# Kernel optimization log

Measured on AMD Instinct MI355X. Metric: run time of the kernel, lower is better.

Reference implementation:

```python
import jax, jax.numpy as jnp
import numpy as np

BETA = 1.0
JITTER = 1e-6


def setup_inputs() -> dict:
    key = jax.random.key(0)
    k1, k2, k3, k4 = jax.random.split(key, 4)
    N, L = 256, 8192
    R_clean = jax.random.normal(k1, (N, L, 3, 3), dtype=jnp.float32)
    t = jax.random.uniform(k2, (N,), dtype=jnp.float32, minval=0.05, maxval=1.0)
    noise = jax.random.normal(k3, (N, L, 3, 3), dtype=jnp.float32)
    eps_noise = jax.random.normal(k4, (N, L, 3, 3), dtype=jnp.float32)
    return {"R_clean": R_clean, "t": t, "noise": noise, "eps_noise": eps_noise}


def _svd_project_so3(F):
    # F: (..., 3, 3).  R = U diag(1,1,det(U V^T)) V^T
    U, S, Vh = jnp.linalg.svd(F, full_matrices=False)
    d = jnp.linalg.det(jnp.matmul(U, Vh))          # (...,)
    mid = jnp.concatenate(
        [jnp.ones(d.shape + (2,), dtype=F.dtype), d[..., None]], axis=-1
    )                                               # (..., 3) = (1, 1, det)
    # U @ diag(mid) @ Vh == (U * mid[..., None, :]) @ Vh
    return jnp.matmul(U * mid[..., None, :], Vh)


def reference(R_clean, t, noise, eps_noise):
    # sample_theta: F_t = alpha_t * R_clean + sqrt(alpha_t) * noise
    alpha_t = (BETA * t).reshape(-1, 1, 1, 1)       # (N,1,1,1)
    F_t = alpha_t * R_clean + jnp.sqrt(alpha_t) * noise
    # svd_project_so3 adds a tiny random jitter before SVD
    F = F_t + JITTER * eps_noise
    return _svd_project_so3(F)
```

## Files before the change

kernel.cpp:

```cpp
#include <hip/hip_runtime.h>

#define TPB  256
#define MPB  256
#define F4PB 576

__device__ __forceinline__ void jrot(float app, float aqq, float apq,
                                     float& c, float& s) {
    float tau = (aqq - app) * 0.5f * __builtin_amdgcn_rcpf(apq);
    float t = __builtin_amdgcn_rcpf(fabsf(tau) +
              __builtin_amdgcn_sqrtf(fmaf(tau, tau, 1.0f)));
    t = copysignf(t, tau);
    t = (fabsf(apq) < 1e-30f) ? 0.0f : t;
    c = __builtin_amdgcn_rsqf(fmaf(t, t, 1.0f));
    s = t * c;
}

__global__ __launch_bounds__(TPB)
void so3_proj_kernel(const float* __restrict__ Rc,
                     const float* __restrict__ Tt,
                     const float* __restrict__ Nz,
                     const float* __restrict__ Ez,
                     float* __restrict__ Out,
                     int L)
{
    __shared__ float4 lds4[F4PB];
    float* lds = (float*)lds4;

    const int tid = threadIdx.x;
    const long long base = (long long)blockIdx.x * MPB;
    const int n = (int)(base / (long long)L);
    const float alpha = Tt[n];
    const float sa = __builtin_amdgcn_sqrtf(alpha);

    const float4* R4 = (const float4*)(Rc + base * 9);
    const float4* N4 = (const float4*)(Nz + base * 9);
    const float4* E4 = (const float4*)(Ez + base * 9);
    float4*       O4 = (float4*)(Out + base * 9);

    #pragma unroll
    for (int it = 0; it < 3; ++it) {
        int j = tid + it * TPB;
        if (j < F4PB) {
            float4 r = R4[j], z = N4[j], e = E4[j];
            float4 f;
            f.x = fmaf(alpha, r.x, fmaf(sa, z.x, 1e-6f * e.x));
            f.y = fmaf(alpha, r.y, fmaf(sa, z.y, 1e-6f * e.y));
            f.z = fmaf(alpha, r.z, fmaf(sa, z.z, 1e-6f * e.z));
            f.w = fmaf(alpha, r.w, fmaf(sa, z.w, 1e-6f * e.w));
            lds4[j] = f;
        }
    }
    __syncthreads();

    float F[9];
    #pragma unroll
    for (int k = 0; k < 9; ++k) F[k] = lds[tid * 9 + k];

    float a00 = F[0]*F[0] + F[3]*F[3] + F[6]*F[6];
    float a01 = F[0]*F[1] + F[3]*F[4] + F[6]*F[7];
    float a02 = F[0]*F[2] + F[3]*F[5] + F[6]*F[8];
    float a11 = F[1]*F[1] + F[4]*F[4] + F[7]*F[7];
    float a12 = F[1]*F[2] + F[4]*F[5] + F[7]*F[8];
    float a22 = F[2]*F[2] + F[5]*F[5] + F[8]*F[8];

    float v00=1.f, v01=0.f, v02=0.f;
    float v10=0.f, v11=1.f, v12=0.f;
    float v20=0.f, v21=0.f, v22=1.f;

    #pragma unroll
    for (int sweep = 0; sweep < 5; ++sweep) {
        float c, s, t0, t1;
        jrot(a00, a11, a01, c, s);
        t0 = c*c*a00 - 2.f*c*s*a01 + s*s*a11;
        t1 = s*s*a00 + 2.f*c*s*a01 + c*c*a11;
        a00 = t0; a11 = t1; a01 = 0.f;
        t0 = c*a02 - s*a12; t1 = s*a02 + c*a12; a02 = t0; a12 = t1;
        t0 = c*v00 - s*v01; v01 = s*v00 + c*v01; v00 = t0;
        t0 = c*v10 - s*v11; v11 = s*v10 + c*v11; v10 = t0;
        t0 = c*v20 - s*v21; v21 = s*v20 + c*v21; v20 = t0;
        jrot(a00, a22, a02, c, s);
        t0 = c*c*a00 - 2.f*c*s*a02 + s*s*a22;
        t1 = s*s*a00 + 2.f*c*s*a02 + c*c*a22;
        a00 = t0; a22 = t1; a02 = 0.f;
        t0 = c*a01 - s*a12; t1 = s*a01 + c*a12; a01 = t0; a12 = t1;
        t0 = c*v00 - s*v02; v02 = s*v00 + c*v02; v00 = t0;
        t0 = c*v10 - s*v12; v12 = s*v10 + c*v12; v10 = t0;
        t0 = c*v20 - s*v22; v22 = s*v20 + c*v22; v20 = t0;
        jrot(a11, a22, a12, c, s);
        t0 = c*c*a11 - 2.f*c*s*a12 + s*s*a22;
        t1 = s*s*a11 + 2.f*c*s*a12 + c*c*a22;
        a11 = t0; a22 = t1; a12 = 0.f;
        t0 = c*a01 - s*a02; t1 = s*a01 + c*a02; a01 = t0; a02 = t1;
        t0 = c*v01 - s*v02; v02 = s*v01 + c*v02; v01 = t0;
        t0 = c*v11 - s*v12; v12 = s*v11 + c*v12; v11 = t0;
        t0 = c*v21 - s*v22; v22 = s*v21 + c*v22; v21 = t0;
    }

    float l0 = a00, l1 = a11, l2 = a22;
    if (l0 < l1) { float t;
        t=l0;l0=l1;l1=t; t=v00;v00=v01;v01=t; t=v10;v10=v11;v11=t; t=v20;v20=v21;v21=t; }
    if (l0 < l2) { float t;
        t=l0;l0=l2;l2=t; t=v00;v00=v02;v02=t; t=v10;v10=v12;v12=t; t=v20;v20=v22;v22=t; }
    if (l1 < l2) { float t;
        t=l1;l1=l2;l2=t; t=v01;v01=v02;v02=t; t=v11;v11=v12;v12=t; t=v21;v21=v22;v22=t; }

    float v3x = v10*v21 - v20*v11;
    float v3y = v20*v01 - v00*v21;
    float v3z = v00*v11 - v10*v01;

    float u1x = F[0]*v00 + F[1]*v10 + F[2]*v20;
    float u1y = F[3]*v00 + F[4]*v10 + F[5]*v20;
    float u1z = F[6]*v00 + F[7]*v10 + F[8]*v20;
    float inv1 = __builtin_amdgcn_rsqf(fmaxf(u1x*u1x + u1y*u1y + u1z*u1z, 1e-30f));
    u1x *= inv1; u1y *= inv1; u1z *= inv1;

    float wx = F[0]*v01 + F[1]*v11 + F[2]*v21;
    float wy = F[3]*v01 + F[4]*v11 + F[5]*v21;
    float wz = F[6]*v01 + F[7]*v11 + F[8]*v21;
    float dd = u1x*wx + u1y*wy + u1z*wz;
    wx -= dd*u1x; wy -= dd*u1y; wz -= dd*u1z;
    float inv2 = __builtin_amdgcn_rsqf(fmaxf(wx*wx + wy*wy + wz*wz, 1e-30f));
    float u2x = wx*inv2, u2y = wy*inv2, u2z = wz*inv2;

    float u3x = u1y*u2z - u1z*u2y;
    float u3y = u1z*u2x - u1x*u2z;
    float u3z = u1x*u2y - u1y*u2x;

    float Rm[9];
    Rm[0] = u1x*v00 + u2x*v01 + u3x*v3x;
    Rm[1] = u1x*v10 + u2x*v11 + u3x*v3y;
    Rm[2] = u1x*v20 + u2x*v21 + u3x*v3z;
    Rm[3] = u1y*v00 + u2y*v01 + u3y*v3x;
    Rm[4] = u1y*v10 + u2y*v11 + u3y*v3y;
    Rm[5] = u1y*v20 + u2y*v21 + u3y*v3z;
    Rm[6] = u1z*v00 + u2z*v01 + u3z*v3x;
    Rm[7] = u1z*v10 + u2z*v11 + u3z*v3y;
    Rm[8] = u1z*v20 + u2z*v21 + u3z*v3z;

    __syncthreads();
    #pragma unroll
    for (int k = 0; k < 9; ++k) lds[tid * 9 + k] = Rm[k];
    __syncthreads();

    #pragma unroll
    for (int it = 0; it < 3; ++it) {
        int j = tid + it * TPB;
        if (j < F4PB) O4[j] = lds4[j];
    }
}

extern "C" void kernel_launch(void* const* d_in, const int* in_sizes, int n_in,
                              void* d_out, int out_size, void* d_ws, size_t ws_size,
                              hipStream_t stream) {
    const float* Rc = (const float*)d_in[0];
    const float* Tt = (const float*)d_in[1];
    const float* Nz = (const float*)d_in[2];
    const float* Ez = (const float*)d_in[3];
    float* Out = (float*)d_out;

    const long long mats = (long long)in_sizes[0] / 9;
    const int L = (int)(mats / in_sizes[1]);
    const int blocks = (int)(mats / MPB);

    so3_proj_kernel<<<blocks, TPB, 0, stream>>>(Rc, Tt, Nz, Ez, Out, L);
}
```

Before: 250.2 us.

## Simplify Jacobi rotations and exit sweeps early on wavefront convergence

Rewrites the Jacobi rotation to compute tan directly from a numerically stable formula with one rcp, and updates the diagonal entries with the a_pp - t*a_pq identity in place of the full quadratic form. It also drops the full unroll of the sweep loop and adds a wavefront-wide convergence test after sweep 3, so waves whose matrices are already diagonal skip the remaining sweeps. The goal is to cut ALU work in a compute-heavy kernel. The trade-offs are an extra reduction and branch per sweep, and the loss of unrolling.

```diff
diff --git a/kernel.cpp b/kernel.cpp
--- a/kernel.cpp
+++ b/kernel.cpp
@@ -5,12 +5,12 @@
 #define F4PB 576
 
 __device__ __forceinline__ void jrot(float app, float aqq, float apq,
-                                     float& c, float& s) {
-    float tau = (aqq - app) * 0.5f * __builtin_amdgcn_rcpf(apq);
-    float t = __builtin_amdgcn_rcpf(fabsf(tau) +
-              __builtin_amdgcn_sqrtf(fmaf(tau, tau, 1.0f)));
-    t = copysignf(t, tau);
-    t = (fabsf(apq) < 1e-30f) ? 0.0f : t;
+                                     float& c, float& s, float& t) {
+    float d  = aqq - app;
+    float p2 = apq + apq;
+    float rad = __builtin_amdgcn_sqrtf(fmaf(d, d, p2 * p2));
+    float den = fmaxf(fabsf(d) + rad, 1e-38f);
+    t = p2 * copysignf(__builtin_amdgcn_rcpf(den), d);
     c = __builtin_amdgcn_rsqf(fmaf(t, t, 1.0f));
     s = t * c;
 }
@@ -67,33 +67,31 @@
     float v10=0.f, v11=1.f, v12=0.f;
     float v20=0.f, v21=0.f, v22=1.f;
 
-    #pragma unroll
     for (int sweep = 0; sweep < 5; ++sweep) {
-        float c, s, t0, t1;
-        jrot(a00, a11, a01, c, s);
-        t0 = c*c*a00 - 2.f*c*s*a01 + s*s*a11;
-        t1 = s*s*a00 + 2.f*c*s*a01 + c*c*a11;
-        a00 = t0; a11 = t1; a01 = 0.f;
-        t0 = c*a02 - s*a12; t1 = s*a02 + c*a12; a02 = t0; a12 = t1;
-        t0 = c*v00 - s*v01; v01 = s*v00 + c*v01; v00 = t0;
-        t0 = c*v10 - s*v11; v11 = s*v10 + c*v11; v10 = t0;
-        t0 = c*v20 - s*v21; v21 = s*v20 + c*v21; v20 = t0;
-        jrot(a00, a22, a02, c, s);
-        t0 = c*c*a00 - 2.f*c*s*a02 + s*s*a22;
-        t1 = s*s*a00 + 2.f*c*s*a02 + c*c*a22;
-        a00 = t0; a22 = t1; a02 = 0.f;
-        t0 = c*a01 - s*a12; t1 = s*a01 + c*a12; a01 = t0; a12 = t1;
-        t0 = c*v00 - s*v02; v02 = s*v00 + c*v02; v00 = t0;
-        t0 = c*v10 - s*v12; v12 = s*v10 + c*v12; v10 = t0;
-        t0 = c*v20 - s*v22; v22 = s*v20 + c*v22; v20 = t0;
-        jrot(a11, a22, a12, c, s);
-        t0 = c*c*a11 - 2.f*c*s*a12 + s*s*a22;
-        t1 = s*s*a11 + 2.f*c*s*a12 + c*c*a22;
-        a11 = t0; a22 = t1; a12 = 0.f;
-        t0 = c*a01 - s*a02; t1 = s*a01 + c*a02; a01 = t0; a02 = t1;
-        t0 = c*v01 - s*v02; v02 = s*v01 + c*v02; v01 = t0;
-        t0 = c*v11 - s*v12; v12 = s*v11 + c*v12; v11 = t0;
-        t0 = c*v21 - s*v22; v22 = s*v21 + c*v22; v21 = t0;
+        if (sweep >= 3) {
+            float off = fmaf(a01, a01, fmaf(a02, a02, a12 * a12));
+            float sc  = fmaf(a00, a00, fmaf(a11, a11, a22 * a22));
+            if (__all(off <= 1e-13f * sc)) break;
+        }
+        float c, s, t, t0;
+        jrot(a00, a11, a01, c, s, t);
+        a00 = fmaf(-t, a01, a00); a11 = fmaf(t, a01, a11); a01 = 0.f;
+        t0 = c*a02 - s*a12; a12 = fmaf(s, a02, c*a12); a02 = t0;
+        t0 = c*v00 - s*v01; v01 = fmaf(s, v00, c*v01); v00 = t0;
+        t0 = c*v10 - s*v11; v11 = fmaf(s, v10, c*v11); v10 = t0;
+        t0 = c*v20 - s*v21; v21 = fmaf(s, v20, c*v21); v20 = t0;
+        jrot(a00, a22, a02, c, s, t);
+        a00 = fmaf(-t, a02, a00); a22 = fmaf(t, a02, a22); a02 = 0.f;
+        t0 = c*a01 - s*a12; a12 = fmaf(s, a01, c*a12); a01 = t0;
+        t0 = c*v00 - s*v02; v02 = fmaf(s, v00, c*v02); v00 = t0;
+        t0 = c*v10 - s*v12; v12 = fmaf(s, v10, c*v12); v10 = t0;
+        t0 = c*v20 - s*v22; v22 = fmaf(s, v20, c*v22); v20 = t0;
+        jrot(a11, a22, a12, c, s, t);
+        a11 = fmaf(-t, a12, a11); a22 = fmaf(t, a12, a22); a12 = 0.f;
+        t0 = c*a01 - s*a02; a02 = fmaf(s, a01, c*a02); a01 = t0;
+        t0 = c*v01 - s*v02; v02 = fmaf(s, v01, c*v02); v01 = t0;
+        t0 = c*v11 - s*v12; v12 = fmaf(s, v11, c*v12); v11 = t0;
+        t0 = c*v21 - s*v22; v22 = fmaf(s, v21, c*v22); v21 = t0;
     }
 
     float l0 = a00, l1 = a11, l2 = a22;
```

After: 244.3 us. 1.02x faster.
